# Performance work log

Measured on AMD Instinct MI355X. Metric: run time of the kernel, lower is better.

Reference implementation:

```python
import jax, jax.numpy as jnp
import numpy as np
import math

B, S, D, H, L, FF, T = 2, 1024, 1024, 16, 8, 4096, 512
HD = D // H
EPS = 1e-5


def _ln(x, g, b):
    m = jnp.mean(x, axis=-1, keepdims=True)
    v = jnp.var(x, axis=-1, keepdims=True)
    return (x - m) * jax.lax.rsqrt(v + EPS) * g + b


def _rope(x, cos, sin):
    # x: [B,S,H,HD]; interleaved even/odd rotary as in _apply_rotary_emb_sincos
    xe, xo = x[..., 0::2], x[..., 1::2]
    c = cos[None, :, None, :]
    s = sin[None, :, None, :]
    return jnp.stack([xe * c - xo * s, xe * s + xo * c], axis=-1).reshape(x.shape)


def setup_inputs():
    key = jax.random.key(0)
    ks = iter(jax.random.split(key, 40))
    n = lambda shape, sc=0.02: jax.random.normal(next(ks), shape, jnp.float32) * sc
    return {
        "inputs_embeds": jax.random.normal(next(ks), (B, S, D), jnp.float32),
        "attention_mask": jnp.ones((B, 1, 1, S), jnp.float32),
        "time_step": jax.random.uniform(next(ks), (B,), jnp.float32),
        "wpe": n((S, D)),
        "ln1_g": jnp.ones((L, D)), "ln1_b": jnp.zeros((L, D)),
        "attn_w": n((L, D, 3 * D)), "attn_b": jnp.zeros((L, 3 * D)),
        "projw": n((L, D, D)), "projb": jnp.zeros((L, D)),
        "ln2_g": jnp.ones((L, D)), "ln2_b": jnp.zeros((L, D)),
        "fcw": n((L, D, FF)), "fcb": jnp.zeros((L, FF)),
        "pw2": n((L, FF, D)), "pb2": jnp.zeros((L, D)),
        "sst": n((L, 6, D), 1.0 / D ** 0.5),
        "te_w1": n((T, D)), "te_b1": jnp.zeros((D,)),
        "te_w2": n((D, D)), "te_b2": jnp.zeros((D,)),
        "ada_w": n((D, 6 * D)), "ada_b": jnp.zeros((6 * D,)),
        "lnf_g": jnp.ones((D,)), "lnf_b": jnp.zeros((D,)),
        "fsst": n((2, D), 1.0 / D ** 0.5),
        "out_w": n((D, D)), "out_b": jnp.zeros((D,)),
    }


def reference(inputs_embeds, attention_mask, time_step, wpe, ln1_g, ln1_b,
              attn_w, attn_b, projw, projb, ln2_g, ln2_b, fcw, fcb, pw2, pb2,
              sst, te_w1, te_b1, te_w2, te_b2, ada_w, ada_b, lnf_g, lnf_b,
              fsst, out_w, out_b):
    hs = inputs_embeds + wpe[:S][None]  # position embedding
    # rotary tables: [S, HD//2]
    half = HD // 2
    freqs = 1.0 / (10000.0 ** (jnp.arange(half, dtype=jnp.float32) * 2.0 / HD))
    ang = jnp.arange(S, dtype=jnp.float32)[:, None] * freqs[None]
    cos, sin = jnp.cos(ang), jnp.sin(ang)
    mask = (1.0 - attention_mask) * jnp.finfo(jnp.float32).min  # [B,1,1,S]
    # timestep embedding (flow_t_size=T, scale=1000, max_period=10000)
    halfT = T // 2
    tf = jnp.exp(-math.log(10000.0) * jnp.arange(halfT, dtype=jnp.float32) / halfT)
    targs = time_step[:, None] * tf[None] * 1000.0
    tproj = jnp.concatenate([jnp.cos(targs), jnp.sin(targs)], axis=-1)  # [B,T]
    emb = jax.nn.silu(tproj @ te_w1 + te_b1) @ te_w2 + te_b2  # [B,D]
    adaln = (jax.nn.silu(emb) @ ada_w + ada_b).reshape(B, 6, D)

    layer_params = dict(ln1_g=ln1_g, ln1_b=ln1_b, aw=attn_w, ab=attn_b,
                        pw=projw, pb=projb, ln2_g=ln2_g, ln2_b=ln2_b,
                        fw=fcw, fb=fcb, qw=pw2, qb=pb2, sst=sst)

    def block(h, p):
        mod = p["sst"][None] + adaln  # [B,6,D]
        sh1, sc1, g1, sh2, sc2, g2 = [mod[:, i:i + 1] for i in range(6)]
        res = h
        x = _ln(h, p["ln1_g"], p["ln1_b"]) * (1.0 + sc1) + sh1
        qkv = x @ p["aw"] + p["ab"]
        q, k, v = [t.reshape(B, S, H, HD) for t in jnp.split(qkv, 3, axis=-1)]
        q, k = _rope(q, cos, sin), _rope(k, cos, sin)
        scores = jnp.einsum("bqhd,bkhd->bhqk", q, k) / math.sqrt(HD) + mask
        attn = jax.nn.softmax(scores, axis=-1)
        o = jnp.einsum("bhqk,bkhd->bqhd", attn, v).reshape(B, S, D)
        o = o @ p["pw"] + p["pb"]
        h = o * g1 + res
        res = h
        x = _ln(h, p["ln2_g"], p["ln2_b"]) * (1.0 + sc2) + sh2
        x = jax.nn.gelu(x @ p["fw"] + p["fb"], approximate=True) @ p["qw"] + p["qb"]
        return x * g2 + res, None

    hs, _ = jax.lax.scan(block, hs, layer_params)
    fmod = fsst[None] + emb[:, None]  # [B,2,D]
    shift, scale = fmod[:, 0:1], fmod[:, 1:2]
    hs = _ln(hs, lnf_g, lnf_b) * (1.0 + scale) + shift
    return hs @ out_w + out_b
```

## Files before the change

kernel.cpp:

```cpp
#include <hip/hip_runtime.h>
#include <stdint.h>

typedef unsigned short u16;
typedef __attribute__((ext_vector_type(8))) short bf8_t;
typedef __attribute__((ext_vector_type(4))) float f4_t;

#define DEV static __device__ __forceinline__
#define MFMA16(a, b, c) __builtin_amdgcn_mfma_f32_16x16x32_bf16((a), (b), (c), 0, 0, 0)
#define GLDS(gp, lp) __builtin_amdgcn_global_load_lds((const __attribute__((address_space(1))) void*)(gp), \
                                                      (__attribute__((address_space(3))) void*)(lp), 16, 0, 0)

DEV u16 f2bf(float f) {
  union { float f; uint32_t u; } x; x.f = f;
  uint32_t r = x.u + 0x7FFFu + ((x.u >> 16) & 1u);
  return (u16)(r >> 16);
}

__global__ __launch_bounds__(256) void transpose_k(const float* __restrict__ W, u16* __restrict__ WT,
                                                   int K, int N) {
  __shared__ float tile[32][33];
  const int n0 = blockIdx.x * 32, k0 = blockIdx.y * 32;
  const int tx = threadIdx.x & 31, ty = threadIdx.x >> 5;
  #pragma unroll
  for (int i = 0; i < 32; i += 8)
    tile[ty + i][tx] = W[(long)(k0 + ty + i) * N + n0 + tx];
  __syncthreads();
  #pragma unroll
  for (int i = 0; i < 32; i += 8)
    WT[(long)(n0 + ty + i) * K + k0 + tx] = f2bf(tile[tx][ty + i]);
}

enum { EPI_F32 = 0, EPI_GATE = 1, EPI_GELU = 2 };

template <int BM, int EPI>
__global__ __launch_bounds__(256)
void gemm_bt(const u16* __restrict__ A, const u16* __restrict__ BT, const float* __restrict__ bias,
             float* outF, u16* outB, const float* gate, const float* res, int M, int N, int K) {
  constexpr int MI = BM / 32;
  __shared__ u16 sA[BM * 32];
  __shared__ u16 sB[128 * 32];
  const int tid = threadIdx.x, lane = tid & 63, wid = tid >> 6;
  const long rowBase = (long)blockIdx.x * BM;
  const long colBase = (long)blockIdx.y * 128;
  const int wr = (wid >> 1) * (BM / 2), wc = (wid & 1) * 64;
  const int fr = lane & 15, kg = (lane >> 4) * 8;

  const f4_t zero = {0.0f, 0.0f, 0.0f, 0.0f};
  f4_t acc[MI][4];
  #pragma unroll
  for (int i = 0; i < MI; ++i)
    #pragma unroll
    for (int j = 0; j < 4; ++j) acc[i][j] = zero;

  const int sr = lane >> 2, scol = (lane & 3) * 8;
  const int c0 = wid * 2;
  const u16 *Ag0, *Ag1 = nullptr, *Bg0, *Bg1;
  u16 *lA0, *lA1 = nullptr, *lB0, *lB1;
  if constexpr (BM == 128) {
    Ag0 = A + (rowBase + c0 * 16 + sr) * (long)K + scol;
    Ag1 = A + (rowBase + c0 * 16 + 16 + sr) * (long)K + scol;
    lA0 = &sA[(c0 * 16) * 32];
    lA1 = &sA[(c0 * 16 + 16) * 32];
  } else {
    Ag0 = A + (rowBase + wid * 16 + sr) * (long)K + scol;
    lA0 = &sA[(wid * 16) * 32];
  }
  Bg0 = BT + (colBase + c0 * 16 + sr) * (long)K + scol;
  Bg1 = BT + (colBase + c0 * 16 + 16 + sr) * (long)K + scol;
  lB0 = &sB[(c0 * 16) * 32];
  lB1 = &sB[(c0 * 16 + 16) * 32];

  for (int k0 = 0; k0 < K; k0 += 32) {
    GLDS(Ag0 + k0, lA0);
    if constexpr (BM == 128) GLDS(Ag1 + k0, lA1);
    GLDS(Bg0 + k0, lB0);
    GLDS(Bg1 + k0, lB1);
    __syncthreads();
    bf8_t af[MI], bfv[4];
    #pragma unroll
    for (int m = 0; m < MI; ++m) af[m] = *(const bf8_t*)&sA[(wr + m * 16 + fr) * 32 + kg];
    #pragma unroll
    for (int n = 0; n < 4; ++n) bfv[n] = *(const bf8_t*)&sB[(wc + n * 16 + fr) * 32 + kg];
    #pragma unroll
    for (int m = 0; m < MI; ++m)
      #pragma unroll
      for (int n = 0; n < 4; ++n) acc[m][n] = MFMA16(af[m], bfv[n], acc[m][n]);
    __syncthreads();
  }

  const int r0 = (lane >> 4) * 4;
  #pragma unroll
  for (int m = 0; m < MI; ++m) {
    #pragma unroll
    for (int n = 0; n < 4; ++n) {
      const long col = colBase + wc + n * 16 + fr;
      const float bv = bias[col];
      #pragma unroll
      for (int j = 0; j < 4; ++j) {
        const long row = rowBase + wr + m * 16 + r0 + j;
        float v = acc[m][n][j] + bv;
        if (EPI == EPI_F32) {
          outF[row * N + col] = v;
        } else if (EPI == EPI_GATE) {
          const int b = (int)(row >> 10);
          const float g = gate[(long)b * 6144 + col];
          outF[row * N + col] = v * g + res[row * N + col];
        } else {
          const float t = 0.7978845608028654f * (v + 0.044715f * v * v * v);
          const float e = __expf(2.0f * t);
          const float th = 1.0f - 2.0f / (e + 1.0f);
          outB[row * N + col] = f2bf(0.5f * v * (1.0f + th));
        }
      }
    }
  }
}

__global__ __launch_bounds__(256)
void ln_mod(const float* __restrict__ h, const float* __restrict__ gamma, const float* __restrict__ beta,
            const float* shp, const float* scp, int bstride, u16* __restrict__ xb) {
  __shared__ float red[8];
  const int row = blockIdx.x;
  const int b = row >> 10;
  const int t = threadIdx.x;
  const float* hp = h + (long)row * 1024;
  float4 x = *(const float4*)&hp[t * 4];
  float s = x.x + x.y + x.z + x.w;
  #pragma unroll
  for (int o = 32; o > 0; o >>= 1) s += __shfl_down(s, o);
  const int lane = t & 63, wid = t >> 6;
  if (lane == 0) red[wid] = s;
  __syncthreads();
  const float mean = (red[0] + red[1] + red[2] + red[3]) * 0.0009765625f;
  const float d0 = x.x - mean, d1 = x.y - mean, d2 = x.z - mean, d3 = x.w - mean;
  float vs = d0 * d0 + d1 * d1 + d2 * d2 + d3 * d3;
  #pragma unroll
  for (int o = 32; o > 0; o >>= 1) vs += __shfl_down(vs, o);
  if (lane == 0) red[4 + wid] = vs;
  __syncthreads();
  const float var = (red[4] + red[5] + red[6] + red[7]) * 0.0009765625f;
  const float inv = rsqrtf(var + 1e-5f);
  const int d = t * 4;
  const float4 gg = *(const float4*)&gamma[d];
  const float4 bb = *(const float4*)&beta[d];
  const float4 sh = *(const float4*)&shp[(long)b * bstride + d];
  const float4 sc = *(const float4*)&scp[(long)b * bstride + d];
  union { u16 u[4]; uint2 v; } pk;
  pk.u[0] = f2bf((d0 * inv * gg.x + bb.x) * (1.0f + sc.x) + sh.x);
  pk.u[1] = f2bf((d1 * inv * gg.y + bb.y) * (1.0f + sc.y) + sh.y);
  pk.u[2] = f2bf((d2 * inv * gg.z + bb.z) * (1.0f + sc.z) + sh.z);
  pk.u[3] = f2bf((d3 * inv * gg.w + bb.w) * (1.0f + sc.w) + sh.w);
  *(uint2*)&xb[(long)row * 1024 + d] = pk.v;
}

__global__ __launch_bounds__(256)
void rope_split(const float* __restrict__ qkv, const float* __restrict__ ct, const float* __restrict__ st,
                u16* __restrict__ qb, u16* __restrict__ kb) {
  const int row = blockIdx.x;
  const int b = row >> 10, s = row & 1023;
  const float* rp = qkv + (long)row * 3072;
  const int t = threadIdx.x;
  #pragma unroll
  for (int which = 0; which < 2; ++which) {
    const float* xp = rp + which * 1024;
    u16* op = which ? kb : qb;
    #pragma unroll
    for (int j = 0; j < 2; ++j) {
      const int p = t + j * 256;
      const int h = p >> 5, i = p & 31;
      const float xe = xp[h * 64 + 2 * i], xo = xp[h * 64 + 2 * i + 1];
      const float c = ct[s * 32 + i], sn = st[s * 32 + i];
      const long base = (((long)(b * 16 + h)) * 1024 + s) * 64 + 2 * i;
      op[base] = f2bf(xe * c - xo * sn);
      op[base + 1] = f2bf(xe * sn + xo * c);
    }
  }
}

__global__ __launch_bounds__(256)
void v_transpose(const float* __restrict__ qkv, u16* __restrict__ vt) {
  __shared__ u16 tile[32][34];
  const int s0 = blockIdx.x * 32;
  const int h = blockIdx.y;
  const int bz = blockIdx.z, b = bz >> 1, dt = bz & 1;
  const int tx = threadIdx.x & 31, ty = threadIdx.x >> 5;
  #pragma unroll
  for (int i = 0; i < 32; i += 8)
    tile[ty + i][tx] = f2bf(qkv[(long)(b * 1024 + s0 + ty + i) * 3072 + 2048 + h * 64 + dt * 32 + tx]);
  __syncthreads();
  #pragma unroll
  for (int i = 0; i < 32; i += 8)
    vt[((long)(b * 16 + h) * 64 + dt * 32 + ty + i) * 1024 + s0 + tx] = tile[tx][ty + i];
}

DEV void attn_body(bf8_t (&kcur)[4][2], bf8_t (&knxt)[4][2], const bf8_t (&qf)[2],
                   f4_t (&oacc)[4], float& m, float& psum, int kc,
                   const u16* __restrict__ Kp, const u16* __restrict__ Vt,
                   const float* smadd, u16* myP, int fr, int g) {
  const f4_t zero = {0.0f, 0.0f, 0.0f, 0.0f};
  bf8_t vf[4][2];
  #pragma unroll
  for (int dt = 0; dt < 4; ++dt)
    #pragma unroll
    for (int ks = 0; ks < 2; ++ks)
      vf[dt][ks] = *(const bf8_t*)&Vt[(long)(dt * 16 + fr) * 1024 + kc + ks * 32 + g * 8];
  f4_t st[4];
  #pragma unroll
  for (int kt = 0; kt < 4; ++kt) {
    st[kt] = MFMA16(kcur[kt][0], qf[0], zero);
    st[kt] = MFMA16(kcur[kt][1], qf[1], st[kt]);
  }
  {
    const int kn = (kc + 64) & 1023;
    #pragma unroll
    for (int kt = 0; kt < 4; ++kt)
      #pragma unroll
      for (int dh = 0; dh < 2; ++dh)
        knxt[kt][dh] = *(const bf8_t*)&Kp[(long)(kn + kt * 16 + fr) * 64 + dh * 32 + g * 8];
  }
  float p[4][4];
  float cm = -3.402823466e38f;
  #pragma unroll
  for (int kt = 0; kt < 4; ++kt)
    #pragma unroll
    for (int j = 0; j < 4; ++j) {
      p[kt][j] = st[kt][j] * 0.125f + smadd[kc + kt * 16 + g * 4 + j];
      cm = fmaxf(cm, p[kt][j]);
    }
  cm = fmaxf(cm, __shfl_xor(cm, 16));
  cm = fmaxf(cm, __shfl_xor(cm, 32));
  const float nm = fmaxf(m, cm);
  const float sc = __expf(m - nm);
  m = nm;
  float ls = 0.0f;
  #pragma unroll
  for (int kt = 0; kt < 4; ++kt)
    #pragma unroll
    for (int j = 0; j < 4; ++j) {
      p[kt][j] = __expf(p[kt][j] - nm);
      ls += p[kt][j];
    }
  psum = psum * sc + ls;
  #pragma unroll
  for (int dt = 0; dt < 4; ++dt)
    #pragma unroll
    for (int j = 0; j < 4; ++j) oacc[dt][j] *= sc;
  #pragma unroll
  for (int kt = 0; kt < 4; ++kt) {
    const int kb = kt * 2 + (g >> 1);
    uint2 w;
    w.x = (uint32_t)f2bf(p[kt][0]) | ((uint32_t)f2bf(p[kt][1]) << 16);
    w.y = (uint32_t)f2bf(p[kt][2]) | ((uint32_t)f2bf(p[kt][3]) << 16);
    *(uint2*)&myP[(kb * 16 + fr) * 8 + (g & 1) * 4] = w;
  }
  bf8_t pa0 = *(const bf8_t*)&myP[(g * 16 + fr) * 8];
  bf8_t pa1 = *(const bf8_t*)&myP[((4 + g) * 16 + fr) * 8];
  #pragma unroll
  for (int dt = 0; dt < 4; ++dt) {
    oacc[dt] = MFMA16(vf[dt][0], pa0, oacc[dt]);
    oacc[dt] = MFMA16(vf[dt][1], pa1, oacc[dt]);
  }
}

__global__ __launch_bounds__(256)
void attn_k(const u16* __restrict__ qb, const u16* __restrict__ kb, const u16* __restrict__ vt,
            const float* __restrict__ amask, u16* __restrict__ ob) {
  __shared__ float smadd[1024];
  __shared__ u16 pl[4][1024];
  const int q0 = blockIdx.x * 64;
  const int h = blockIdx.y, b = blockIdx.z;
  const long bh = b * 16 + h;
  const int tid = threadIdx.x, lane = tid & 63, wid = tid >> 6;
  const int fr = lane & 15, g = lane >> 4;

  for (int i = tid; i < 1024; i += 256)
    smadd[i] = (1.0f - amask[b * 1024 + i]) * -3.402823466e38f;
  __syncthreads();

  const u16* Q = qb + (bh * 1024 + q0 + wid * 16) * 64;
  const u16* Kp = kb + bh * 1024 * 64;
  const u16* Vt = vt + bh * 64 * 1024;
  u16* myP = &pl[wid][0];

  bf8_t qf[2];
  qf[0] = *(const bf8_t*)&Q[fr * 64 + g * 8];
  qf[1] = *(const bf8_t*)&Q[fr * 64 + 32 + g * 8];

  const f4_t zero = {0.0f, 0.0f, 0.0f, 0.0f};
  f4_t oacc[4];
  #pragma unroll
  for (int dt = 0; dt < 4; ++dt) oacc[dt] = zero;
  float m = -1e30f, psum = 0.0f;

  bf8_t kfA[4][2], kfB[4][2];
  #pragma unroll
  for (int kt = 0; kt < 4; ++kt)
    #pragma unroll
    for (int dh = 0; dh < 2; ++dh)
      kfA[kt][dh] = *(const bf8_t*)&Kp[(long)(kt * 16 + fr) * 64 + dh * 32 + g * 8];

  for (int kc = 0; kc < 1024; kc += 128) {
    attn_body(kfA, kfB, qf, oacc, m, psum, kc, Kp, Vt, smadd, myP, fr, g);
    attn_body(kfB, kfA, qf, oacc, m, psum, kc + 64, Kp, Vt, smadd, myP, fr, g);
  }

  float ts = psum + __shfl_xor(psum, 16);
  ts += __shfl_xor(ts, 32);
  const float inv = 1.0f / ts;
  const long qrow = (long)b * 1024 + q0 + wid * 16 + fr;
  #pragma unroll
  for (int dt = 0; dt < 4; ++dt) {
    union { u16 u[4]; uint2 v; } pk;
    #pragma unroll
    for (int j = 0; j < 4; ++j) pk.u[j] = f2bf(oacc[dt][j] * inv);
    *(uint2*)&ob[qrow * 1024 + h * 64 + dt * 16 + g * 4] = pk.v;
  }
}

__global__ void rope_tables(float* ct, float* st) {
  const int i = blockIdx.x * 256 + threadIdx.x;
  const int s = i >> 5, k = i & 31;
  const float freq = __expf(-9.210340371976184f * (float)(2 * k) / 64.0f);
  const float a = (float)s * freq;
  ct[i] = cosf(a);
  st[i] = sinf(a);
}

__global__ void init_hs(const float* __restrict__ e, const float* __restrict__ wpe, float* __restrict__ hs) {
  const long i = (long)blockIdx.x * 256 + threadIdx.x;
  float4 a = ((const float4*)e)[i];
  const float4 w = ((const float4*)wpe)[i & 262143];
  a.x += w.x; a.y += w.y; a.z += w.z; a.w += w.w;
  ((float4*)hs)[i] = a;
}

__global__ void time_proj_k(const float* __restrict__ ts, float* __restrict__ tproj) {
  const int j = blockIdx.x * 256 + threadIdx.x;
  const int b = blockIdx.y;
  const float tf = __expf(-9.210340371976184f * (float)(j & 255) / 256.0f);
  const float a = ts[b] * tf * 1000.0f;
  tproj[b * 512 + j] = (j < 256) ? cosf(a) : sinf(a);
}

__global__ void time_mlp1(const float* __restrict__ tproj, const float* __restrict__ w1,
                          const float* __restrict__ b1, float* __restrict__ h1) {
  const int d = blockIdx.x * 256 + threadIdx.x;
  const int b = blockIdx.y;
  float acc = b1[d];
  for (int j = 0; j < 512; ++j) acc += tproj[b * 512 + j] * w1[(long)j * 1024 + d];
  h1[b * 1024 + d] = acc / (1.0f + __expf(-acc));
}

__global__ void time_mlp2(const float* __restrict__ h1, const float* __restrict__ w2,
                          const float* __restrict__ b2, float* __restrict__ emb) {
  const int d = blockIdx.x * 256 + threadIdx.x;
  const int b = blockIdx.y;
  float acc = b2[d];
  for (int j = 0; j < 1024; ++j) acc += h1[b * 1024 + j] * w2[(long)j * 1024 + d];
  emb[b * 1024 + d] = acc;
}

__global__ void silu_k(const float* __restrict__ in, float* __restrict__ out, int n) {
  const int i = blockIdx.x * 256 + threadIdx.x;
  if (i < n) { const float v = in[i]; out[i] = v / (1.0f + __expf(-v)); }
}

__global__ void adaln_k(const float* __restrict__ se, const float* __restrict__ aw,
                        const float* __restrict__ ab, float* __restrict__ adaln) {
  const int j = blockIdx.x * 256 + threadIdx.x;
  const int b = blockIdx.y;
  float acc = ab[j];
  for (int k = 0; k < 1024; ++k) acc += se[b * 1024 + k] * aw[(long)k * 6144 + j];
  adaln[b * 6144 + j] = acc;
}

__global__ void build_mods(const float* __restrict__ sst, const float* __restrict__ adaln,
                           const float* __restrict__ fsst, const float* __restrict__ emb,
                           float* __restrict__ modAll, float* __restrict__ fmod) {
  const int i = blockIdx.x * 256 + threadIdx.x;
  if (i < 98304) {
    const int d = i & 1023;
    const int rest = i >> 10;
    const int slot = rest % 6;
    const int t2 = rest / 6;
    const int bb = t2 & 1, l = t2 >> 1;
    modAll[i] = sst[(long)(l * 6 + slot) * 1024 + d] + adaln[bb * 6144 + slot * 1024 + d];
  } else if (i < 98304 + 4096) {
    const int j = i - 98304;
    const int d = j & 1023;
    const int slot = (j >> 10) & 1;
    const int bb = j >> 11;
    fmod[j] = fsst[slot * 1024 + d] + emb[bb * 1024 + d];
  }
}

extern "C" void kernel_launch(void* const* d_in, const int* in_sizes, int n_in,
                              void* d_out, int out_size, void* d_ws, size_t ws_size,
                              hipStream_t stream) {
  const float* inp_emb = (const float*)d_in[0];
  const float* amask  = (const float*)d_in[1];
  const float* tstep  = (const float*)d_in[2];
  const float* wpe    = (const float*)d_in[3];
  const float* ln1_g  = (const float*)d_in[4];
  const float* ln1_b  = (const float*)d_in[5];
  const float* attn_w = (const float*)d_in[6];
  const float* attn_b = (const float*)d_in[7];
  const float* projw  = (const float*)d_in[8];
  const float* projb  = (const float*)d_in[9];
  const float* ln2_g  = (const float*)d_in[10];
  const float* ln2_b  = (const float*)d_in[11];
  const float* fcw    = (const float*)d_in[12];
  const float* fcb    = (const float*)d_in[13];
  const float* pw2    = (const float*)d_in[14];
  const float* pb2    = (const float*)d_in[15];
  const float* sst    = (const float*)d_in[16];
  const float* te_w1  = (const float*)d_in[17];
  const float* te_b1  = (const float*)d_in[18];
  const float* te_w2  = (const float*)d_in[19];
  const float* te_b2  = (const float*)d_in[20];
  const float* ada_w  = (const float*)d_in[21];
  const float* ada_b  = (const float*)d_in[22];
  const float* lnf_g  = (const float*)d_in[23];
  const float* lnf_b  = (const float*)d_in[24];
  const float* fsst   = (const float*)d_in[25];
  const float* out_w  = (const float*)d_in[26];
  const float* out_b  = (const float*)d_in[27];
  float* out = (float*)d_out;
  (void)in_sizes; (void)n_in; (void)out_size; (void)ws_size;

  char* wsb = (char*)d_ws;
  size_t off = 0;
  auto alloc = [&](size_t bytes) -> void* {
    void* p = wsb + off;
    off += (bytes + 255) & ~(size_t)255;
    return p;
  };
  u16* wtA = (u16*)alloc(3072ll * 1024 * 2);
  u16* wtP = (u16*)alloc(1024ll * 1024 * 2);
  u16* wtF = (u16*)alloc(4096ll * 1024 * 2);
  u16* wtQ = (u16*)alloc(1024ll * 4096 * 2);
  u16* wtO = (u16*)alloc(1024ll * 1024 * 2);
  float* hs   = (float*)alloc(2048ll * 1024 * 4);
  float* qkv  = (float*)alloc(2048ll * 3072 * 4);
  u16*   ffb  = (u16*)qkv;
  u16* xb = (u16*)alloc(2048ll * 1024 * 2);
  u16* qb = (u16*)alloc(2048ll * 1024 * 2);
  u16* kb = (u16*)alloc(2048ll * 1024 * 2);
  u16* vt = (u16*)alloc(2048ll * 1024 * 2);
  u16* ob = (u16*)alloc(2048ll * 1024 * 2);
  float* ct    = (float*)alloc(32768 * 4);
  float* st    = (float*)alloc(32768 * 4);
  float* tproj = (float*)alloc(2 * 512 * 4);
  float* h1    = (float*)alloc(2 * 1024 * 4);
  float* emb   = (float*)alloc(2 * 1024 * 4);
  float* se    = (float*)alloc(2 * 1024 * 4);
  float* adaln = (float*)alloc(2 * 6144 * 4);
  float* modAll = (float*)alloc(8ll * 2 * 6 * 1024 * 4);
  float* fmod   = (float*)alloc(2 * 2 * 1024 * 4);

  rope_tables<<<128, 256, 0, stream>>>(ct, st);
  init_hs<<<2048, 256, 0, stream>>>(inp_emb, wpe, hs);
  time_proj_k<<<dim3(2, 2), 256, 0, stream>>>(tstep, tproj);
  time_mlp1<<<dim3(4, 2), 256, 0, stream>>>(tproj, te_w1, te_b1, h1);
  time_mlp2<<<dim3(4, 2), 256, 0, stream>>>(h1, te_w2, te_b2, emb);
  silu_k<<<8, 256, 0, stream>>>(emb, se, 2048);
  adaln_k<<<dim3(24, 2), 256, 0, stream>>>(se, ada_w, ada_b, adaln);
  build_mods<<<400, 256, 0, stream>>>(sst, adaln, fsst, emb, modAll, fmod);
  transpose_k<<<dim3(32, 32), 256, 0, stream>>>(out_w, wtO, 1024, 1024);

  for (int l = 0; l < 8; ++l) {
    const float* ml = modAll + (long)l * 12288;
    transpose_k<<<dim3(96, 32), 256, 0, stream>>>(attn_w + (long)l * 1024 * 3072, wtA, 1024, 3072);
    transpose_k<<<dim3(32, 32), 256, 0, stream>>>(projw + (long)l * 1024 * 1024, wtP, 1024, 1024);
    transpose_k<<<dim3(128, 32), 256, 0, stream>>>(fcw + (long)l * 1024 * 4096, wtF, 1024, 4096);
    transpose_k<<<dim3(32, 128), 256, 0, stream>>>(pw2 + (long)l * 4096 * 1024, wtQ, 4096, 1024);

    ln_mod<<<2048, 256, 0, stream>>>(hs, ln1_g + l * 1024, ln1_b + l * 1024,
                                     ml + 0 * 1024, ml + 1 * 1024, 6144, xb);
    gemm_bt<128, EPI_F32><<<dim3(16, 24), 256, 0, stream>>>(xb, wtA, attn_b + l * 3072,
                                                            qkv, nullptr, nullptr, nullptr, 2048, 3072, 1024);
    rope_split<<<2048, 256, 0, stream>>>(qkv, ct, st, qb, kb);
    v_transpose<<<dim3(32, 16, 4), 256, 0, stream>>>(qkv, vt);
    attn_k<<<dim3(16, 16, 2), 256, 0, stream>>>(qb, kb, vt, amask, ob);
    gemm_bt<64, EPI_GATE><<<dim3(32, 8), 256, 0, stream>>>(ob, wtP, projb + l * 1024,
                                                           hs, nullptr, ml + 2 * 1024, hs, 2048, 1024, 1024);
    ln_mod<<<2048, 256, 0, stream>>>(hs, ln2_g + l * 1024, ln2_b + l * 1024,
                                     ml + 3 * 1024, ml + 4 * 1024, 6144, xb);
    gemm_bt<128, EPI_GELU><<<dim3(16, 32), 256, 0, stream>>>(xb, wtF, fcb + l * 4096,
                                                             nullptr, ffb, nullptr, nullptr, 2048, 4096, 1024);
    gemm_bt<64, EPI_GATE><<<dim3(32, 8), 256, 0, stream>>>(ffb, wtQ, pb2 + l * 1024,
                                                           hs, nullptr, ml + 5 * 1024, hs, 2048, 1024, 4096);
  }

  ln_mod<<<2048, 256, 0, stream>>>(hs, lnf_g, lnf_b, fmod + 0, fmod + 1024, 2048, xb);
  gemm_bt<64, EPI_F32><<<dim3(32, 8), 256, 0, stream>>>(xb, wtO, out_b,
                                                        out, nullptr, nullptr, nullptr, 2048, 1024, 1024);
}
```

Before: 2.259 ms.

## Vectorize transposes, merge weight transposes, split-K FFN down-proj, parallelize time MLPs

Weight and V transposes now use 64x64 bf16 tiles with float4 loads and 8-byte stores, and the four per-layer weight transposes are merged into one launch. The FFN down-projection becomes a split-K GEMM (BM=128, two K halves) writing fp32 partials, followed by a reduce kernel that adds bias, applies the gate and adds the residual. The time-embedding MLPs and the adaLN projection are spread over more blocks with in-block or split-K reductions. These changes target low memory efficiency and low occupancy, at the cost of an extra partial buffer and extra reduce traffic.

```diff
diff --git a/kernel.cpp b/kernel.cpp
--- a/kernel.cpp
+++ b/kernel.cpp
@@ -16,23 +16,54 @@
   return (u16)(r >> 16);
 }
 
+DEV void transpose_body(const float* __restrict__ W, u16* __restrict__ WT, int K, int N,
+                        int n0, int k0, u16 (*tl)[66]) {
+  const int t = threadIdx.x;
+  const int tx = t & 15, ty = t >> 4;
+  #pragma unroll
+  for (int i = 0; i < 64; i += 16) {
+    const float4 v = *(const float4*)&W[(long)(k0 + ty + i) * N + n0 + tx * 4];
+    tl[tx * 4 + 0][ty + i] = f2bf(v.x);
+    tl[tx * 4 + 1][ty + i] = f2bf(v.y);
+    tl[tx * 4 + 2][ty + i] = f2bf(v.z);
+    tl[tx * 4 + 3][ty + i] = f2bf(v.w);
+  }
+  __syncthreads();
+  const int c = t & 15, r = t >> 4;
+  #pragma unroll
+  for (int i = 0; i < 64; i += 16) {
+    const u16* p = &tl[r + i][c * 4];
+    uint2 w;
+    w.x = (uint32_t)p[0] | ((uint32_t)p[1] << 16);
+    w.y = (uint32_t)p[2] | ((uint32_t)p[3] << 16);
+    *(uint2*)&WT[(long)(n0 + r + i) * K + k0 + c * 4] = w;
+  }
+}
+
 __global__ __launch_bounds__(256) void transpose_k(const float* __restrict__ W, u16* __restrict__ WT,
                                                    int K, int N) {
-  __shared__ float tile[32][33];
-  const int n0 = blockIdx.x * 32, k0 = blockIdx.y * 32;
-  const int tx = threadIdx.x & 31, ty = threadIdx.x >> 5;
-  #pragma unroll
-  for (int i = 0; i < 32; i += 8)
-    tile[ty + i][tx] = W[(long)(k0 + ty + i) * N + n0 + tx];
-  __syncthreads();
-  #pragma unroll
-  for (int i = 0; i < 32; i += 8)
-    WT[(long)(n0 + ty + i) * K + k0 + tx] = f2bf(tile[tx][ty + i]);
-}
-
-enum { EPI_F32 = 0, EPI_GATE = 1, EPI_GELU = 2 };
-
-template <int BM, int EPI>
+  __shared__ u16 tl[64][66];
+  transpose_body(W, WT, K, N, blockIdx.x * 64, blockIdx.y * 64, tl);
+}
+
+__global__ __launch_bounds__(256)
+void transpose4_k(const float* __restrict__ w0, u16* __restrict__ o0,
+                  const float* __restrict__ w1, u16* __restrict__ o1,
+                  const float* __restrict__ w2, u16* __restrict__ o2,
+                  const float* __restrict__ w3, u16* __restrict__ o3) {
+  __shared__ u16 tl[64][66];
+  int bid = blockIdx.x;
+  const float* W; u16* O; int K, N, nbx;
+  if (bid < 768)        {             W = w0; O = o0; K = 1024; N = 3072; nbx = 48; }
+  else if (bid < 1024)  { bid -= 768; W = w1; O = o1; K = 1024; N = 1024; nbx = 16; }
+  else if (bid < 2048)  { bid -= 1024; W = w2; O = o2; K = 1024; N = 4096; nbx = 64; }
+  else                  { bid -= 2048; W = w3; O = o3; K = 4096; N = 1024; nbx = 16; }
+  transpose_body(W, O, K, N, (bid % nbx) * 64, (bid / nbx) * 64, tl);
+}
+
+enum { EPI_F32 = 0, EPI_GATE = 1, EPI_GELU = 2, EPI_RAW = 3 };
+
+template <int BM, int EPI, int KS>
 __global__ __launch_bounds__(256)
 void gemm_bt(const u16* __restrict__ A, const u16* __restrict__ BT, const float* __restrict__ bias,
              float* outF, u16* outB, const float* gate, const float* res, int M, int N, int K) {
@@ -42,6 +73,8 @@
   const int tid = threadIdx.x, lane = tid & 63, wid = tid >> 6;
   const long rowBase = (long)blockIdx.x * BM;
   const long colBase = (long)blockIdx.y * 128;
+  const int kz = (KS > 1) ? blockIdx.z : 0;
+  const int kbeg = kz * (K / KS), kend = kbeg + K / KS;
   const int wr = (wid >> 1) * (BM / 2), wc = (wid & 1) * 64;
   const int fr = lane & 15, kg = (lane >> 4) * 8;
 
@@ -70,7 +103,7 @@
   lB0 = &sB[(c0 * 16) * 32];
   lB1 = &sB[(c0 * 16 + 16) * 32];
 
-  for (int k0 = 0; k0 < K; k0 += 32) {
+  for (int k0 = kbeg; k0 < kend; k0 += 32) {
     GLDS(Ag0 + k0, lA0);
     if constexpr (BM == 128) GLDS(Ag1 + k0, lA1);
     GLDS(Bg0 + k0, lB0);
@@ -94,13 +127,15 @@
     #pragma unroll
     for (int n = 0; n < 4; ++n) {
       const long col = colBase + wc + n * 16 + fr;
-      const float bv = bias[col];
+      const float bv = (EPI == EPI_RAW) ? 0.0f : bias[col];
       #pragma unroll
       for (int j = 0; j < 4; ++j) {
         const long row = rowBase + wr + m * 16 + r0 + j;
         float v = acc[m][n][j] + bv;
         if (EPI == EPI_F32) {
           outF[row * N + col] = v;
+        } else if (EPI == EPI_RAW) {
+          outF[((long)kz * M + row) * N + col] = v;
         } else if (EPI == EPI_GATE) {
           const int b = (int)(row >> 10);
           const float g = gate[(long)b * 6144 + col];
@@ -114,6 +149,25 @@
       }
     }
   }
+}
+
+__global__ __launch_bounds__(256)
+void reduce_gate(const float* __restrict__ part, const float* __restrict__ bias,
+                 const float* __restrict__ gate, float* __restrict__ hs) {
+  const long i = (long)blockIdx.x * 256 + threadIdx.x;
+  const long e0 = i * 4;
+  const int col = (int)(e0 & 1023);
+  const int row = (int)(e0 >> 10);
+  const int b = row >> 10;
+  const f4_t p = *(const f4_t*)&part[e0];
+  const f4_t q = *(const f4_t*)&part[e0 + 2048ll * 1024];
+  const f4_t bv = *(const f4_t*)&bias[col];
+  const f4_t gv = *(const f4_t*)&gate[(long)b * 6144 + col];
+  const f4_t r = *(const f4_t*)&hs[e0];
+  f4_t o;
+  #pragma unroll
+  for (int j = 0; j < 4; ++j) o[j] = (p[j] + q[j] + bv[j]) * gv[j] + r[j];
+  *(f4_t*)&hs[e0] = o;
 }
 
 __global__ __launch_bounds__(256)
@@ -179,18 +233,29 @@
 
 __global__ __launch_bounds__(256)
 void v_transpose(const float* __restrict__ qkv, u16* __restrict__ vt) {
-  __shared__ u16 tile[32][34];
-  const int s0 = blockIdx.x * 32;
-  const int h = blockIdx.y;
-  const int bz = blockIdx.z, b = bz >> 1, dt = bz & 1;
-  const int tx = threadIdx.x & 31, ty = threadIdx.x >> 5;
-  #pragma unroll
-  for (int i = 0; i < 32; i += 8)
-    tile[ty + i][tx] = f2bf(qkv[(long)(b * 1024 + s0 + ty + i) * 3072 + 2048 + h * 64 + dt * 32 + tx]);
-  __syncthreads();
-  #pragma unroll
-  for (int i = 0; i < 32; i += 8)
-    vt[((long)(b * 16 + h) * 64 + dt * 32 + ty + i) * 1024 + s0 + tx] = tile[tx][ty + i];
+  __shared__ u16 tl[64][66];
+  const int s0 = blockIdx.x * 64;
+  const int h = blockIdx.y, b = blockIdx.z;
+  const int t = threadIdx.x;
+  const int tx = t & 15, ty = t >> 4;
+  #pragma unroll
+  for (int i = 0; i < 64; i += 16) {
+    const float4 v = *(const float4*)&qkv[(long)(b * 1024 + s0 + ty + i) * 3072 + 2048 + h * 64 + tx * 4];
+    tl[tx * 4 + 0][ty + i] = f2bf(v.x);
+    tl[tx * 4 + 1][ty + i] = f2bf(v.y);
+    tl[tx * 4 + 2][ty + i] = f2bf(v.z);
+    tl[tx * 4 + 3][ty + i] = f2bf(v.w);
+  }
+  __syncthreads();
+  const int c = t & 15, r = t >> 4;
+  #pragma unroll
+  for (int i = 0; i < 64; i += 16) {
+    const u16* p = &tl[r + i][c * 4];
+    uint2 w;
+    w.x = (uint32_t)p[0] | ((uint32_t)p[1] << 16);
+    w.y = (uint32_t)p[2] | ((uint32_t)p[3] << 16);
+    *(uint2*)&vt[((long)(b * 16 + h) * 64 + r + i) * 1024 + s0 + c * 4] = w;
+  }
 }
 
 DEV void attn_body(bf8_t (&kcur)[4][2], bf8_t (&knxt)[4][2], const bf8_t (&qf)[2],
@@ -342,22 +407,42 @@
   tproj[b * 512 + j] = (j < 256) ? cosf(a) : sinf(a);
 }
 
-__global__ void time_mlp1(const float* __restrict__ tproj, const float* __restrict__ w1,
-                          const float* __restrict__ b1, float* __restrict__ h1) {
-  const int d = blockIdx.x * 256 + threadIdx.x;
-  const int b = blockIdx.y;
-  float acc = b1[d];
-  for (int j = 0; j < 512; ++j) acc += tproj[b * 512 + j] * w1[(long)j * 1024 + d];
-  h1[b * 1024 + d] = acc / (1.0f + __expf(-acc));
-}
-
-__global__ void time_mlp2(const float* __restrict__ h1, const float* __restrict__ w2,
-                          const float* __restrict__ b2, float* __restrict__ emb) {
-  const int d = blockIdx.x * 256 + threadIdx.x;
-  const int b = blockIdx.y;
-  float acc = b2[d];
-  for (int j = 0; j < 1024; ++j) acc += h1[b * 1024 + j] * w2[(long)j * 1024 + d];
-  emb[b * 1024 + d] = acc;
+__global__ __launch_bounds__(256)
+void time_mlp1(const float* __restrict__ tproj, const float* __restrict__ w1,
+               const float* __restrict__ b1, float* __restrict__ h1) {
+  __shared__ float red[8][32];
+  const int dl = threadIdx.x & 31, sl = threadIdx.x >> 5;
+  const int d = blockIdx.x * 32 + dl, b = blockIdx.y;
+  float acc = 0.0f;
+  for (int j = sl * 64; j < sl * 64 + 64; ++j) acc += tproj[b * 512 + j] * w1[(long)j * 1024 + d];
+  red[sl][dl] = acc;
+  __syncthreads();
+  if (threadIdx.x < 32) {
+    const int dd = blockIdx.x * 32 + threadIdx.x;
+    float a = b1[dd];
+    #pragma unroll
+    for (int s = 0; s < 8; ++s) a += red[s][threadIdx.x];
+    h1[b * 1024 + dd] = a / (1.0f + __expf(-a));
+  }
+}
+
+__global__ __launch_bounds__(256)
+void time_mlp2(const float* __restrict__ h1, const float* __restrict__ w2,
+               const float* __restrict__ b2, float* __restrict__ emb) {
+  __shared__ float red[8][32];
+  const int dl = threadIdx.x & 31, sl = threadIdx.x >> 5;
+  const int d = blockIdx.x * 32 + dl, b = blockIdx.y;
+  float acc = 0.0f;
+  for (int j = sl * 128; j < sl * 128 + 128; ++j) acc += h1[b * 1024 + j] * w2[(long)j * 1024 + d];
+  red[sl][dl] = acc;
+  __syncthreads();
+  if (threadIdx.x < 32) {
+    const int dd = blockIdx.x * 32 + threadIdx.x;
+    float a = b2[dd];
+    #pragma unroll
+    for (int s = 0; s < 8; ++s) a += red[s][threadIdx.x];
+    emb[b * 1024 + dd] = a;
+  }
 }
 
 __global__ void silu_k(const float* __restrict__ in, float* __restrict__ out, int n) {
@@ -365,12 +450,22 @@
   if (i < n) { const float v = in[i]; out[i] = v / (1.0f + __expf(-v)); }
 }
 
-__global__ void adaln_k(const float* __restrict__ se, const float* __restrict__ aw,
-                        const float* __restrict__ ab, float* __restrict__ adaln) {
+__global__ void adaln_part(const float* __restrict__ se, const float* __restrict__ aw,
+                           float* __restrict__ part) {
+  const int j = blockIdx.x * 256 + threadIdx.x;
+  const int b = blockIdx.y, kz = blockIdx.z;
+  float acc = 0.0f;
+  for (int k = kz * 128; k < kz * 128 + 128; ++k) acc += se[b * 1024 + k] * aw[(long)k * 6144 + j];
+  part[((long)kz * 2 + b) * 6144 + j] = acc;
+}
+
+__global__ void adaln_reduce(const float* __restrict__ part, const float* __restrict__ ab,
+                             float* __restrict__ adaln) {
   const int j = blockIdx.x * 256 + threadIdx.x;
   const int b = blockIdx.y;
   float acc = ab[j];
-  for (int k = 0; k < 1024; ++k) acc += se[b * 1024 + k] * aw[(long)k * 6144 + j];
+  #pragma unroll
+  for (int kz = 0; kz < 8; ++kz) acc += part[((long)kz * 2 + b) * 6144 + j];
   adaln[b * 6144 + j] = acc;
 }
 
@@ -443,6 +538,7 @@
   float* hs   = (float*)alloc(2048ll * 1024 * 4);
   float* qkv  = (float*)alloc(2048ll * 3072 * 4);
   u16*   ffb  = (u16*)qkv;
+  float* part = (float*)alloc(2ll * 2048 * 1024 * 4);
   u16* xb = (u16*)alloc(2048ll * 1024 * 2);
   u16* qb = (u16*)alloc(2048ll * 1024 * 2);
   u16* kb = (u16*)alloc(2048ll * 1024 * 2);
@@ -461,38 +557,40 @@
   rope_tables<<<128, 256, 0, stream>>>(ct, st);
   init_hs<<<2048, 256, 0, stream>>>(inp_emb, wpe, hs);
   time_proj_k<<<dim3(2, 2), 256, 0, stream>>>(tstep, tproj);
-  time_mlp1<<<dim3(4, 2), 256, 0, stream>>>(tproj, te_w1, te_b1, h1);
-  time_mlp2<<<dim3(4, 2), 256, 0, stream>>>(h1, te_w2, te_b2, emb);
+  time_mlp1<<<dim3(32, 2), 256, 0, stream>>>(tproj, te_w1, te_b1, h1);
+  time_mlp2<<<dim3(32, 2), 256, 0, stream>>>(h1, te_w2, te_b2, emb);
   silu_k<<<8, 256, 0, stream>>>(emb, se, 2048);
-  adaln_k<<<dim3(24, 2), 256, 0, stream>>>(se, ada_w, ada_b, adaln);
+  adaln_part<<<dim3(24, 2, 8), 256, 0, stream>>>(se, ada_w, part);
+  adaln_reduce<<<dim3(24, 2), 256, 0, stream>>>(part, ada_b, adaln);
   build_mods<<<400, 256, 0, stream>>>(sst, adaln, fsst, emb, modAll, fmod);
-  transpose_k<<<dim3(32, 32), 256, 0, stream>>>(out_w, wtO, 1024, 1024);
+  transpose_k<<<dim3(16, 16), 256, 0, stream>>>(out_w, wtO, 1024, 1024);
 
   for (int l = 0; l < 8; ++l) {
     const float* ml = modAll + (long)l * 12288;
-    transpose_k<<<dim3(96, 32), 256, 0, stream>>>(attn_w + (long)l * 1024 * 3072, wtA, 1024, 3072);
-    transpose_k<<<dim3(32, 32), 256, 0, stream>>>(projw + (long)l * 1024 * 1024, wtP, 1024, 1024);
-    transpose_k<<<dim3(128, 32), 256, 0, stream>>>(fcw + (long)l * 1024 * 4096, wtF, 1024, 4096);
-    transpose_k<<<dim3(32, 128), 256, 0, stream>>>(pw2 + (long)l * 4096 * 1024, wtQ, 4096, 1024);
+    transpose4_k<<<3072, 256, 0, stream>>>(attn_w + (long)l * 1024 * 3072, wtA,
+                                           projw + (long)l * 1024 * 1024, wtP,
+                                           fcw + (long)l * 1024 * 4096, wtF,
+                                           pw2 + (long)l * 4096 * 1024, wtQ);
 
     ln_mod<<<2048, 256, 0, stream>>>(hs, ln1_g + l * 1024, ln1_b + l * 1024,
                                      ml + 0 * 1024, ml + 1 * 1024, 6144, xb);
-    gemm_bt<128, EPI_F32><<<dim3(16, 24), 256, 0, stream>>>(xb, wtA, attn_b + l * 3072,
-                                                            qkv, nullptr, nullptr, nullptr, 2048, 3072, 1024);
+    gemm_bt<128, EPI_F32, 1><<<dim3(16, 24), 256, 0, stream>>>(xb, wtA, attn_b + l * 3072,
+                                                               qkv, nullptr, nullptr, nullptr, 2048, 3072, 1024);
     rope_split<<<2048, 256, 0, stream>>>(qkv, ct, st, qb, kb);
-    v_transpose<<<dim3(32, 16, 4), 256, 0, stream>>>(qkv, vt);
+    v_transpose<<<dim3(16, 16, 2), 256, 0, stream>>>(qkv, vt);
     attn_k<<<dim3(16, 16, 2), 256, 0, stream>>>(qb, kb, vt, amask, ob);
-    gemm_bt<64, EPI_GATE><<<dim3(32, 8), 256, 0, stream>>>(ob, wtP, projb + l * 1024,
-                                                           hs, nullptr, ml + 2 * 1024, hs, 2048, 1024, 1024);
+    gemm_bt<64, EPI_GATE, 1><<<dim3(32, 8), 256, 0, stream>>>(ob, wtP, projb + l * 1024,
+                                                              hs, nullptr, ml + 2 * 1024, hs, 2048, 1024, 1024);
     ln_mod<<<2048, 256, 0, stream>>>(hs, ln2_g + l * 1024, ln2_b + l * 1024,
                                      ml + 3 * 1024, ml + 4 * 1024, 6144, xb);
-    gemm_bt<128, EPI_GELU><<<dim3(16, 32), 256, 0, stream>>>(xb, wtF, fcb + l * 4096,
-                                                             nullptr, ffb, nullptr, nullptr, 2048, 4096, 1024);
-    gemm_bt<64, EPI_GATE><<<dim3(32, 8), 256, 0, stream>>>(ffb, wtQ, pb2 + l * 1024,
-                                                           hs, nullptr, ml + 5 * 1024, hs, 2048, 1024, 4096);
+    gemm_bt<128, EPI_GELU, 1><<<dim3(16, 32), 256, 0, stream>>>(xb, wtF, fcb + l * 4096,
+                                                                nullptr, ffb, nullptr, nullptr, 2048, 4096, 1024);
+    gemm_bt<128, EPI_RAW, 2><<<dim3(16, 8, 2), 256, 0, stream>>>(ffb, wtQ, nullptr,
+                                                                 part, nullptr, nullptr, nullptr, 2048, 1024, 4096);
+    reduce_gate<<<2048, 256, 0, stream>>>(part, pb2 + l * 1024, ml + 5 * 1024, hs);
   }
 
   ln_mod<<<2048, 256, 0, stream>>>(hs, lnf_g, lnf_b, fmod + 0, fmod + 1024, 2048, xb);
-  gemm_bt<64, EPI_F32><<<dim3(32, 8), 256, 0, stream>>>(xb, wtO, out_b,
-                                                        out, nullptr, nullptr, nullptr, 2048, 1024, 1024);
-}
+  gemm_bt<64, EPI_F32, 1><<<dim3(32, 8), 256, 0, stream>>>(xb, wtO, out_b,
+                                                           out, nullptr, nullptr, nullptr, 2048, 1024, 1024);
+}
```

Measured after the change: 1.951 ms. -13.6%, faster.
